# Kernel tuning notes

Hardware: AMD Instinct MI355X
Metric: run time of the kernel (lower is better)

Reference implementation:

```python
import jax, jax.numpy as jnp
import numpy as np

C = 512
GROUPS = 8
EPS = 1e-5


def setup_inputs() -> dict:
    key = jax.random.key(0)
    ks = jax.random.split(key, 7)
    B, H, W = 16, 32, 32
    x = jax.random.normal(ks[0], (B, C, H, W), dtype=jnp.float32)
    # GroupNorm affine params
    gn_scale = jnp.ones((C,), jnp.float32)
    gn_bias = jnp.zeros((C,), jnp.float32)
    # 1x1 convs == channel matmuls
    s_qkv = 1.0 / np.sqrt(C)
    qkv_w = jax.random.uniform(ks[1], (3 * C, C), jnp.float32, -s_qkv, s_qkv)
    qkv_b = jax.random.uniform(ks[2], (3 * C,), jnp.float32, -s_qkv, s_qkv)
    proj_w = jax.random.uniform(ks[3], (C, C), jnp.float32, -s_qkv, s_qkv)
    proj_b = jax.random.uniform(ks[4], (C,), jnp.float32, -s_qkv, s_qkv)
    return {"x": x, "gn_scale": gn_scale, "gn_bias": gn_bias,
            "qkv_w": qkv_w, "qkv_b": qkv_b, "proj_w": proj_w, "proj_b": proj_b}


def _group_norm(x, scale, bias):
    B, c, H, W = x.shape
    xg = x.reshape(B, GROUPS, c // GROUPS, H, W)
    mean = xg.mean(axis=(2, 3, 4), keepdims=True)
    var = xg.var(axis=(2, 3, 4), keepdims=True)
    xn = ((xg - mean) * jax.lax.rsqrt(var + EPS)).reshape(B, c, H, W)
    return xn * scale[None, :, None, None] + bias[None, :, None, None]


def reference(x, gn_scale, gn_bias, qkv_w, qkv_b, proj_w, proj_b):
    B, c, H, W = x.shape
    N = H * W
    h = _group_norm(x, gn_scale, gn_bias)            # [B,C,H,W]
    hf = h.reshape(B, c, N)                          # flatten spatial
    qkv = jnp.einsum('oc,bcn->bon', qkv_w, hf) + qkv_b[None, :, None]  # [B,3C,N]
    q, k, v = jnp.split(qkv, 3, axis=1)              # each [B,C,N]
    attn = jnp.einsum('bci,bcj->bij', q, k) * (c ** -0.5)  # [B,N,N]
    attn = jax.nn.softmax(attn, axis=2)
    out = jnp.einsum('bij,bcj->bci', attn, v)        # [B,C,N]
    out = jnp.einsum('oc,bcn->bon', proj_w, out) + proj_b[None, :, None]
    return out.reshape(B, c, H, W) + x
```

## Files before the change

kernel.cpp:

```cpp
#include <hip/hip_runtime.h>

typedef __bf16 bf16x8 __attribute__((ext_vector_type(8)));
typedef float f32x4 __attribute__((ext_vector_type(4)));
typedef unsigned short u16;

__device__ __forceinline__ u16 f2bf(float f) {
  unsigned u = __float_as_uint(f);
  u += 0x7fffu + ((u >> 16) & 1u);
  return (u16)(u >> 16);
}
__device__ __forceinline__ float bf2f(u16 h) {
  return __uint_as_float(((unsigned)h) << 16);
}

#define GLOAD_LDS(g, l)                                              \
  __builtin_amdgcn_global_load_lds(                                  \
      (const __attribute__((address_space(1))) void*)(g),            \
      (__attribute__((address_space(3))) void*)(l), 16, 0, 0)

template <int K>
__device__ __forceinline__ void gemm_core_s(const u16* __restrict__ Ab,
                                            const u16* __restrict__ Bb,
                                            f32x4 acc[4][4]) {
  __shared__ __align__(16) u16 As[8192], Bs[8192];
  const int tid = threadIdx.x;
  const int wave = tid >> 6, lane = tid & 63;
  const int sr = tid >> 3;
  const int sc = ((tid ^ sr) & 7) << 3;
  const u16* ag = Ab + (size_t)sr * K + sc;
  const u16* bg = Bb + (size_t)sr * K + sc;
  u16* al = As + tid * 8;
  u16* bl = Bs + tid * 8;
  const int wr = (wave >> 1) << 6, wc = (wave & 1) << 6;
  const int lrow = lane & 15, klane = lane >> 4;
  const int rx = lrow & 7;
  const int ao = (wr + lrow) * 64 + ((klane ^ rx) << 3);
  const int bo = (wc + lrow) * 64 + ((klane ^ rx) << 3);

  for (int k = 0; k < K; k += 64) {
    __syncthreads();
#pragma unroll
    for (int r = 0; r < 4; r++)
      GLOAD_LDS(ag + (size_t)(r * 32) * K + k, al + r * 2048);
#pragma unroll
    for (int r = 0; r < 4; r++)
      GLOAD_LDS(bg + (size_t)(r * 32) * K + k, bl + r * 2048);
    __syncthreads();
#pragma unroll
    for (int half = 0; half < 2; half++) {
      const int xo = half << 5;
      bf16x8 a[4], b[4];
#pragma unroll
      for (int i = 0; i < 4; i++) a[i] = *(const bf16x8*)(As + ((ao ^ xo) + (i << 10)));
#pragma unroll
      for (int i = 0; i < 4; i++) b[i] = *(const bf16x8*)(Bs + ((bo ^ xo) + (i << 10)));
#pragma unroll
      for (int mi = 0; mi < 4; mi++)
#pragma unroll
        for (int ni = 0; ni < 4; ni++)
          acc[mi][ni] = __builtin_amdgcn_mfma_f32_16x16x32_bf16(a[mi], b[ni], acc[mi][ni], 0, 0, 0);
    }
  }
}

#define ACC_INIT                                     \
  f32x4 acc[4][4];                                   \
  {                                                  \
    const f32x4 _z = {0.f, 0.f, 0.f, 0.f};           \
    _Pragma("unroll")                                \
    for (int _i = 0; _i < 4; _i++)                   \
      _Pragma("unroll")                              \
      for (int _j = 0; _j < 4; _j++) acc[_i][_j] = _z; \
  }

#define EPI_SETUP                                                            \
  const int tid = threadIdx.x;                                               \
  const int wave = tid >> 6;                                                 \
  const int lane = tid & 63;                                                 \
  const int mb = (blockIdx.y << 7) + ((wave >> 1) << 6) + (((lane >> 4) & 3) << 2); \
  const int nb = (blockIdx.x << 7) + ((wave & 1) << 6) + (lane & 15);

__global__ void __launch_bounds__(256) k_convw(const float* __restrict__ qw,
                                               const float* __restrict__ pw,
                                               u16* __restrict__ wq, u16* __restrict__ wp) {
  const int t = blockIdx.x * 256 + threadIdx.x;
  for (int i = t; i < 786432; i += 262144) wq[i] = f2bf(qw[i]);
  wp[t] = f2bf(pw[t]);
}

__global__ void __launch_bounds__(256) k_gn(const float* __restrict__ x,
                                            const float* __restrict__ gsc,
                                            const float* __restrict__ gbi,
                                            u16* __restrict__ h) {
  const int b = blockIdx.x >> 3, g = blockIdx.x & 7;
  const size_t xoff = ((size_t)b * 512 + g * 64) * 1024;
  const float* xb = x + xoff;
  const int tid = threadIdx.x;
  const int wave = tid >> 6, lane = tid & 63;

  float s1 = 0.f, s2 = 0.f;
  const float4* xb4 = (const float4*)xb;
  for (int i = tid; i < 16384; i += 256) {
    float4 v = xb4[i];
    s1 += v.x + v.y + v.z + v.w;
    s2 += v.x * v.x + v.y * v.y + v.z * v.z + v.w * v.w;
  }
#pragma unroll
  for (int off = 32; off; off >>= 1) { s1 += __shfl_xor(s1, off); s2 += __shfl_xor(s2, off); }
  __shared__ float red[8];
  if (lane == 0) { red[wave] = s1; red[4 + wave] = s2; }
  __syncthreads();
  const float t1 = red[0] + red[1] + red[2] + red[3];
  const float t2 = red[4] + red[5] + red[6] + red[7];
  const float mean = t1 * (1.f / 65536.f);
  const float rstd = rsqrtf(t2 * (1.f / 65536.f) - mean * mean + 1e-5f);

  __shared__ u16 tile[64][66];
  for (int chunk = 0; chunk < 16; chunk++) {
    const int n0 = chunk << 6;
    __syncthreads();
#pragma unroll
    for (int r = 0; r < 16; r++) {
      const int cl = (r << 2) + wave;
      const int ch = (g << 6) + cl;
      float v = xb[(size_t)cl * 1024 + n0 + lane];
      float o = (v - mean) * rstd * gsc[ch] + gbi[ch];
      tile[lane][cl] = f2bf(o);
    }
    __syncthreads();
#pragma unroll
    for (int r = 0; r < 16; r++) {
      const int nl = (r << 2) + wave;
      h[((size_t)b * 1024 + n0 + nl) * 512 + (g << 6) + lane] = tile[nl][lane];
    }
  }
}

__global__ void __launch_bounds__(256) k_qkv(const u16* __restrict__ W,
                                             const u16* __restrict__ h,
                                             const float* __restrict__ bias,
                                             u16* __restrict__ qt, u16* __restrict__ kt,
                                             u16* __restrict__ vv) {
  const int b = blockIdx.z;
  ACC_INIT
  gemm_core_s<512>(W + ((size_t)blockIdx.y << 7) * 512,
                   h + ((size_t)b << 19) + (((size_t)blockIdx.x << 7) * 512), acc);
  EPI_SETUP
  const int sel = blockIdx.y >> 2;
  const float scale = 0.044194173824159216f;
  if (sel < 2) {
    u16* dst = sel ? kt : qt;
    const float sc = sel ? 1.f : scale;
    const int obase = mb - sel * 512;
#pragma unroll
    for (int mi = 0; mi < 4; mi++) {
      const int o = mb + mi * 16;
#pragma unroll
      for (int ni = 0; ni < 4; ni++) {
        const int n = nb + ni * 16;
        ushort4 pk;
        pk.x = f2bf((acc[mi][ni][0] + bias[o + 0]) * sc);
        pk.y = f2bf((acc[mi][ni][1] + bias[o + 1]) * sc);
        pk.z = f2bf((acc[mi][ni][2] + bias[o + 2]) * sc);
        pk.w = f2bf((acc[mi][ni][3] + bias[o + 3]) * sc);
        *(ushort4*)(dst + ((size_t)b * 1024 + n) * 512 + (obase + mi * 16)) = pk;
      }
    }
  } else {
#pragma unroll
    for (int mi = 0; mi < 4; mi++) {
      const int o = mb + mi * 16;
#pragma unroll
      for (int ni = 0; ni < 4; ni++) {
        const int n = nb + ni * 16;
#pragma unroll
        for (int r = 0; r < 4; r++) {
          float val = acc[mi][ni][r] + bias[o + r];
          vv[((size_t)b * 512 + (o - 1024 + r)) * 1024 + n] = f2bf(val);
        }
      }
    }
  }
}

__global__ void __launch_bounds__(256) k_sgemm(const u16* __restrict__ qt,
                                               const u16* __restrict__ kt,
                                               u16* __restrict__ S) {
  const int b = blockIdx.z;
  ACC_INIT
  gemm_core_s<512>(qt + ((size_t)b << 19) + ((size_t)blockIdx.y << 7) * 512,
                   kt + ((size_t)b << 19) + ((size_t)blockIdx.x << 7) * 512, acc);
  EPI_SETUP
  const size_t base = (size_t)b << 20;
#pragma unroll
  for (int mi = 0; mi < 4; mi++)
#pragma unroll
    for (int ni = 0; ni < 4; ni++) {
      const int j = nb + ni * 16;
#pragma unroll
      for (int r = 0; r < 4; r++)
        S[base + (size_t)(mb + mi * 16 + r) * 1024 + j] = f2bf(acc[mi][ni][r]);
    }
}

__global__ void __launch_bounds__(256) k_softmax(u16* __restrict__ S) {
  const size_t base = (((size_t)blockIdx.y << 10) + blockIdx.x) << 10;
  const int tid = threadIdx.x;
  const int wave = tid >> 6, lane = tid & 63;
  ushort4 raw = *(const ushort4*)(S + base + tid * 4);
  float v0 = bf2f(raw.x), v1 = bf2f(raw.y), v2 = bf2f(raw.z), v3 = bf2f(raw.w);
  float m = fmaxf(fmaxf(v0, v1), fmaxf(v2, v3));
#pragma unroll
  for (int off = 32; off; off >>= 1) m = fmaxf(m, __shfl_xor(m, off));
  __shared__ float s1[4], s2[4];
  if (lane == 0) s1[wave] = m;
  __syncthreads();
  m = fmaxf(fmaxf(s1[0], s1[1]), fmaxf(s1[2], s1[3]));
  v0 = __expf(v0 - m); v1 = __expf(v1 - m); v2 = __expf(v2 - m); v3 = __expf(v3 - m);
  float s = v0 + v1 + v2 + v3;
#pragma unroll
  for (int off = 32; off; off >>= 1) s += __shfl_xor(s, off);
  if (lane == 0) s2[wave] = s;
  __syncthreads();
  s = s2[0] + s2[1] + s2[2] + s2[3];
  const float inv = 1.0f / s;
  raw.x = f2bf(v0 * inv); raw.y = f2bf(v1 * inv);
  raw.z = f2bf(v2 * inv); raw.w = f2bf(v3 * inv);
  *(ushort4*)(S + base + tid * 4) = raw;
}

__global__ void __launch_bounds__(256) k_ogemm(const u16* __restrict__ vv,
                                               const u16* __restrict__ P,
                                               u16* __restrict__ ot) {
  const int b = blockIdx.z;
  ACC_INIT
  gemm_core_s<1024>(vv + ((size_t)b << 19) + ((size_t)blockIdx.y << 7) * 1024,
                    P + ((size_t)b << 20) + ((size_t)blockIdx.x << 7) * 1024, acc);
  EPI_SETUP
#pragma unroll
  for (int mi = 0; mi < 4; mi++) {
    const int c = mb + mi * 16;
#pragma unroll
    for (int ni = 0; ni < 4; ni++) {
      const int i = nb + ni * 16;
      ushort4 pk;
      pk.x = f2bf(acc[mi][ni][0]);
      pk.y = f2bf(acc[mi][ni][1]);
      pk.z = f2bf(acc[mi][ni][2]);
      pk.w = f2bf(acc[mi][ni][3]);
      *(ushort4*)(ot + ((size_t)b << 19) + (size_t)i * 512 + c) = pk;
    }
  }
}

__global__ void __launch_bounds__(256) k_proj(const u16* __restrict__ W,
                                              const u16* __restrict__ ot,
                                              const float* __restrict__ pb,
                                              const float* __restrict__ x,
                                              float* __restrict__ out) {
  const int b = blockIdx.z;
  ACC_INIT
  gemm_core_s<512>(W + ((size_t)blockIdx.y << 7) * 512,
                   ot + ((size_t)b << 19) + ((size_t)blockIdx.x << 7) * 512, acc);
  EPI_SETUP
#pragma unroll
  for (int mi = 0; mi < 4; mi++) {
    const int o = mb + mi * 16;
#pragma unroll
    for (int ni = 0; ni < 4; ni++) {
      const int n = nb + ni * 16;
      const size_t base = ((size_t)b * 512 + o) * 1024 + n;
#pragma unroll
      for (int r = 0; r < 4; r++)
        out[base + (size_t)r * 1024] = acc[mi][ni][r] + pb[o + r] + x[base + (size_t)r * 1024];
    }
  }
}

extern "C" void kernel_launch(void* const* d_in, const int* in_sizes, int n_in,
                              void* d_out, int out_size, void* d_ws, size_t ws_size,
                              hipStream_t stream) {
  const float* x     = (const float*)d_in[0];
  const float* gsc   = (const float*)d_in[1];
  const float* gbi   = (const float*)d_in[2];
  const float* qkvw  = (const float*)d_in[3];
  const float* qkvb  = (const float*)d_in[4];
  const float* projw = (const float*)d_in[5];
  const float* projb = (const float*)d_in[6];
  float* out = (float*)d_out;

  char* ws = (char*)d_ws;
  u16* wq = (u16*)(ws);
  u16* wp = (u16*)(ws + 1572864);
  u16* h  = (u16*)(ws + 2097152);
  u16* qt = (u16*)(ws + 18874368);
  u16* kt = (u16*)(ws + 35651584);
  u16* vv = (u16*)(ws + 52428864);
  u16* S  = (u16*)(ws + 69206080);
  u16* ot = h;

  k_convw<<<1024, 256, 0, stream>>>(qkvw, projw, wq, wp);
  k_gn<<<128, 256, 0, stream>>>(x, gsc, gbi, h);
  k_qkv<<<dim3(8, 12, 16), 256, 0, stream>>>(wq, h, qkvb, qt, kt, vv);
  k_sgemm<<<dim3(8, 8, 16), 256, 0, stream>>>(qt, kt, S);
  k_softmax<<<dim3(1024, 16), 256, 0, stream>>>(S);
  k_ogemm<<<dim3(8, 4, 16), 256, 0, stream>>>(vv, S, ot);
  k_proj<<<dim3(8, 4, 16), 256, 0, stream>>>(wp, ot, projb, x, out);
}
```

Measured before the change: 293.3 us.

## Double-buffer LDS tiles in GEMM core to overlap loads with MFMA

The shared GEMM core now uses two LDS buffers per operand and issues the global-to-LDS loads for the next k-tile before computing on the current one. This removes one barrier per iteration and overlaps memory latency with matrix-core work. The cost is doubled LDS usage per block, which may lower occupancy.

```diff
diff --git a/kernel.cpp b/kernel.cpp
--- a/kernel.cpp
+++ b/kernel.cpp
@@ -22,44 +22,70 @@
 __device__ __forceinline__ void gemm_core_s(const u16* __restrict__ Ab,
                                             const u16* __restrict__ Bb,
                                             f32x4 acc[4][4]) {
-  __shared__ __align__(16) u16 As[8192], Bs[8192];
+  __shared__ __align__(16) u16 As[2][8192], Bs[2][8192];
   const int tid = threadIdx.x;
   const int wave = tid >> 6, lane = tid & 63;
   const int sr = tid >> 3;
   const int sc = ((tid ^ sr) & 7) << 3;
   const u16* ag = Ab + (size_t)sr * K + sc;
   const u16* bg = Bb + (size_t)sr * K + sc;
-  u16* al = As + tid * 8;
-  u16* bl = Bs + tid * 8;
+  const int ldst = tid * 8;
   const int wr = (wave >> 1) << 6, wc = (wave & 1) << 6;
   const int lrow = lane & 15, klane = lane >> 4;
   const int rx = lrow & 7;
   const int ao = (wr + lrow) * 64 + ((klane ^ rx) << 3);
   const int bo = (wc + lrow) * 64 + ((klane ^ rx) << 3);
 
-  for (int k = 0; k < K; k += 64) {
-    __syncthreads();
-#pragma unroll
-    for (int r = 0; r < 4; r++)
-      GLOAD_LDS(ag + (size_t)(r * 32) * K + k, al + r * 2048);
-#pragma unroll
-    for (int r = 0; r < 4; r++)
-      GLOAD_LDS(bg + (size_t)(r * 32) * K + k, bl + r * 2048);
-    __syncthreads();
+  const u16 *a_cur = As[0] + ldst, *a_nxt = As[1] + ldst;
+  const u16 *b_cur = Bs[0] + ldst, *b_nxt = Bs[1] + ldst;
+  const u16 *ar = As[0], *br = Bs[0];
+  const u16 *an = As[1], *bn = Bs[1];
+
+#pragma unroll
+  for (int r = 0; r < 4; r++) GLOAD_LDS(ag + (size_t)(r * 32) * K, a_cur + r * 2048);
+#pragma unroll
+  for (int r = 0; r < 4; r++) GLOAD_LDS(bg + (size_t)(r * 32) * K, b_cur + r * 2048);
+  __syncthreads();
+
+  for (int k = 64; k < K; k += 64) {
+#pragma unroll
+    for (int r = 0; r < 4; r++) GLOAD_LDS(ag + (size_t)(r * 32) * K + k, a_nxt + r * 2048);
+#pragma unroll
+    for (int r = 0; r < 4; r++) GLOAD_LDS(bg + (size_t)(r * 32) * K + k, b_nxt + r * 2048);
 #pragma unroll
     for (int half = 0; half < 2; half++) {
       const int xo = half << 5;
       bf16x8 a[4], b[4];
 #pragma unroll
-      for (int i = 0; i < 4; i++) a[i] = *(const bf16x8*)(As + ((ao ^ xo) + (i << 10)));
-#pragma unroll
-      for (int i = 0; i < 4; i++) b[i] = *(const bf16x8*)(Bs + ((bo ^ xo) + (i << 10)));
+      for (int i = 0; i < 4; i++) a[i] = *(const bf16x8*)(ar + ((ao ^ xo) + (i << 10)));
+#pragma unroll
+      for (int i = 0; i < 4; i++) b[i] = *(const bf16x8*)(br + ((bo ^ xo) + (i << 10)));
 #pragma unroll
       for (int mi = 0; mi < 4; mi++)
 #pragma unroll
         for (int ni = 0; ni < 4; ni++)
           acc[mi][ni] = __builtin_amdgcn_mfma_f32_16x16x32_bf16(a[mi], b[ni], acc[mi][ni], 0, 0, 0);
     }
+    __syncthreads();
+    const u16* t;
+    t = a_cur; a_cur = a_nxt; a_nxt = t;
+    t = b_cur; b_cur = b_nxt; b_nxt = t;
+    t = ar; ar = an; an = t;
+    t = br; br = bn; bn = t;
+  }
+#pragma unroll
+  for (int half = 0; half < 2; half++) {
+    const int xo = half << 5;
+    bf16x8 a[4], b[4];
+#pragma unroll
+    for (int i = 0; i < 4; i++) a[i] = *(const bf16x8*)(ar + ((ao ^ xo) + (i << 10)));
+#pragma unroll
+    for (int i = 0; i < 4; i++) b[i] = *(const bf16x8*)(br + ((bo ^ xo) + (i << 10)));
+#pragma unroll
+    for (int mi = 0; mi < 4; mi++)
+#pragma unroll
+      for (int ni = 0; ni < 4; ni++)
+        acc[mi][ni] = __builtin_amdgcn_mfma_f32_16x16x32_bf16(a[mi], b[ni], acc[mi][ni], 0, 0, 0);
   }
 }
 
```

New measurement: 268.5 us. -8.5%, faster.
